# Optimization experiments

Hardware: AMD Instinct MI355X
Metric: run time of the kernel (lower is better)

## Reference

```python
import jax, jax.numpy as jnp
import numpy as np

B, K, D = 512, 36, 1024
N_KERNELS = 4
OUT_DIM = 1024
OUT_PER_KERNEL = OUT_DIM // N_KERNELS  # 256


def setup_inputs() -> dict:
    key = jax.random.key(0)
    k1, k2, k3, k4, k5 = jax.random.split(key, 5)
    neighbourhood_features = jax.random.normal(k1, (B, K, D), dtype=jnp.float32)
    region_relation_weights = jax.random.uniform(k2, (B, K, K), dtype=jnp.float32)
    # Gaussian mixture params: init uniform(0, 1) as in init_parameters()
    mean_relation = jax.random.uniform(k3, (N_KERNELS,), dtype=jnp.float32)
    precision_relation = jax.random.uniform(k4, (N_KERNELS,), dtype=jnp.float32)
    # Per-kernel Linear weights (bias=False), torch default init U(-1/sqrt(D), 1/sqrt(D))
    bound = 1.0 / np.sqrt(D)
    W = jax.random.uniform(k5, (N_KERNELS, OUT_PER_KERNEL, D), dtype=jnp.float32,
                           minval=-bound, maxval=bound)
    return {
        "neighbourhood_features": neighbourhood_features,
        "region_relation_weights": region_relation_weights,
        "mean_relation": mean_relation,
        "precision_relation": precision_relation,
        "W": W,
    }


def reference(neighbourhood_features, region_relation_weights, mean_relation,
              precision_relation, W):
    b, k, d = neighbourhood_features.shape
    # Gaussian mixture edge weights, normalized over kernels: [B,K,K,n_kernels]
    diff = (region_relation_weights[..., None] - mean_relation) ** 2
    w = jnp.exp(-0.5 * diff / (1e-14 + precision_relation ** 2))
    w = w / jnp.sum(w, axis=-1, keepdims=True)
    # Original repeats feat[b,i] over the neighbour axis j, so
    # bmm(w^T, repeated_feat)[b,i,k,:] == (sum_j w[b,i,j,k]) * feat[b,i,:].
    # Exploit that linearity instead of materializing the [B,K,K,D] repeat.
    ws = jnp.sum(w, axis=2)  # [B,K,n_kernels]
    weighted = ws[..., None] * neighbourhood_features[:, :, None, :]  # [B,K,n,D]
    # Per-kernel linear (stacked): [B,K,n_kernels,out_per_kernel]
    out = jnp.einsum('bknd,nod->bkno', weighted, W)
    # Concatenate kernel outputs -> [B,K,out_feat_dim]
    return out.reshape(b, k, -1)
```

## Files before the change

kernel.cpp:

```cpp
#include <hip/hip_runtime.h>
#include <stdint.h>

#define BB   512
#define KNB  36
#define DD   1024
#define MM   (BB*KNB)
#define NN   1024

typedef float  f32x4  __attribute__((ext_vector_type(4)));
typedef __bf16 bf16x8 __attribute__((ext_vector_type(8)));
typedef unsigned short u16;
typedef unsigned int   u32;

__device__ __forceinline__ u16 f2bf(float f) {
    u32 u = __float_as_uint(f);
    u32 r = (u + 0x7fffu + ((u >> 16) & 1u)) >> 16;
    return (u16)r;
}

__device__ __forceinline__ void gld16(const void* g, void* l) {
    __builtin_amdgcn_global_load_lds(
        (const __attribute__((address_space(1))) u32*)g,
        (__attribute__((address_space(3))) u32*)l,
        16, 0, 0);
}

__device__ __forceinline__ void cast_chunk_swz(const float* __restrict__ in,
                                               u16* __restrict__ out,
                                               long long c, int r) {
    long long src = (c & ~7LL) | ((c & 7) ^ (r & 7));
    const f32x4* p = (const f32x4*)(in + src * 8);
    f32x4 v0 = p[0], v1 = p[1];
    union { u16 us[8]; uint4 u4; } pk;
    pk.us[0] = f2bf(v0.x); pk.us[1] = f2bf(v0.y);
    pk.us[2] = f2bf(v0.z); pk.us[3] = f2bf(v0.w);
    pk.us[4] = f2bf(v1.x); pk.us[5] = f2bf(v1.y);
    pk.us[6] = f2bf(v1.z); pk.us[7] = f2bf(v1.w);
    *((uint4*)(out + c * 8)) = pk.u4;
}

#define WS_BLOCKS   72
#define CW_BLOCKS   512
#define CA_BLOCKS   1152
#define CA_THREADS  (CA_BLOCKS * 256)
__global__ void prep_kernel(const float* __restrict__ rrw,
                            const float* __restrict__ mean,
                            const float* __restrict__ prec,
                            float* __restrict__ wsT,
                            const float* __restrict__ W,
                            u16* __restrict__ Wbf,
                            const float* __restrict__ A,
                            u16* __restrict__ Abf) {
    const int blk = blockIdx.x;
    if (blk < WS_BLOCKS) {
        int id = blk * 256 + threadIdx.x;
        float m0 = mean[0], m1 = mean[1], m2 = mean[2], m3 = mean[3];
        float i0 = 1.0f / (1e-14f + prec[0] * prec[0]);
        float i1 = 1.0f / (1e-14f + prec[1] * prec[1]);
        float i2 = 1.0f / (1e-14f + prec[2] * prec[2]);
        float i3 = 1.0f / (1e-14f + prec[3] * prec[3]);
        const float* p = rrw + (size_t)id * KNB;
        float a0 = 0.f, a1 = 0.f, a2 = 0.f, a3 = 0.f;
        for (int j = 0; j < KNB; ++j) {
            float x = p[j];
            float d0 = x - m0, d1 = x - m1, d2 = x - m2, d3 = x - m3;
            float e0 = expf(-0.5f * d0 * d0 * i0);
            float e1 = expf(-0.5f * d1 * d1 * i1);
            float e2 = expf(-0.5f * d2 * d2 * i2);
            float e3 = expf(-0.5f * d3 * d3 * i3);
            float inv = 1.0f / (e0 + e1 + e2 + e3);
            a0 += e0 * inv; a1 += e1 * inv; a2 += e2 * inv; a3 += e3 * inv;
        }
        wsT[0 * MM + id] = a0;
        wsT[1 * MM + id] = a1;
        wsT[2 * MM + id] = a2;
        wsT[3 * MM + id] = a3;
    } else if (blk < WS_BLOCKS + CW_BLOCKS) {
        long long c = (long long)(blk - WS_BLOCKS) * 256 + threadIdx.x;
        int r = (int)(c >> 7);
        cast_chunk_swz(W, Wbf, c, r);
    } else {
        long long t = (long long)(blk - WS_BLOCKS - CW_BLOCKS) * 256 + threadIdx.x;
#pragma unroll
        for (int k = 0; k < 8; ++k) {
            long long c = t + (long long)k * CA_THREADS;
            int r = (int)(c >> 7);
            cast_chunk_swz(A, Abf, c, r);
        }
    }
}

#define BM 128
#define BN 128
#define BK 64
#define KTILES (DD / BK)

__global__ __launch_bounds__(256, 4) void gemm_kernel(
        const u16* __restrict__ A,
        const u16* __restrict__ Bm,
        const float* __restrict__ wsT,
        float* __restrict__ out) {
    __shared__ __align__(16) u16 As[BM * BK];
    __shared__ __align__(16) u16 Bs[BN * BK];

    const int tid = threadIdx.x;
    const int bid   = blockIdx.x;
    const int xcd   = bid & 7;
    const int local = bid >> 3;
    const int by    = xcd * 18 + (local >> 3);
    const int bx    = local & 7;
    const int rowBase = by * BM;
    const int colBase = bx * BN;
    const int lane = tid & 63;
    const int w    = tid >> 6;
    const int wr   = w >> 1;
    const int wc   = w & 1;
    const int fr   = lane & 15;
    const int fq   = lane >> 4;

    f32x4 acc[4][4];
#pragma unroll
    for (int m = 0; m < 4; ++m)
#pragma unroll
        for (int n = 0; n < 4; ++n)
            acc[m][n] = (f32x4)0.0f;

    const u16* aptr = A  + (size_t)(rowBase + (tid >> 3)) * DD + (tid & 7) * 8;
    const u16* bptr = Bm + (size_t)(colBase + (tid >> 3)) * DD + (tid & 7) * 8;

    for (int kt = 0; kt < KTILES; ++kt) {
        if (kt) __syncthreads();
#pragma unroll
        for (int i = 0; i < 4; ++i) {
            gld16(aptr + (size_t)i * 32 * DD + kt * BK, &As[(i * 256 + tid) * 8]);
            gld16(bptr + (size_t)i * 32 * DD + kt * BK, &Bs[(i * 256 + tid) * 8]);
        }
        __syncthreads();

#pragma unroll
        for (int kk = 0; kk < 2; ++kk) {
            bf16x8 af[4], bfv[4];
#pragma unroll
            for (int m = 0; m < 4; ++m) {
                int r = wr * 64 + m * 16 + fr;
                int g = kk * 4 + fq;
                af[m] = ((const bf16x8*)&As[r * BK])[g ^ (r & 7)];
            }
#pragma unroll
            for (int n = 0; n < 4; ++n) {
                int r = wc * 64 + n * 16 + fr;
                int g = kk * 4 + fq;
                bfv[n] = ((const bf16x8*)&Bs[r * BK])[g ^ (r & 7)];
            }
#pragma unroll
            for (int m = 0; m < 4; ++m)
#pragma unroll
                for (int n = 0; n < 4; ++n)
                    acc[m][n] = __builtin_amdgcn_mfma_f32_16x16x32_bf16(
                        af[m], bfv[n], acc[m][n], 0, 0, 0);
        }
    }

    const int kn = bx >> 1;
#pragma unroll
    for (int m = 0; m < 4; ++m) {
        int r0 = rowBase + wr * 64 + m * 16 + fq * 4;
        f32x4 s = *(const f32x4*)&wsT[(size_t)kn * MM + r0];
#pragma unroll
        for (int n = 0; n < 4; ++n) {
            int c = colBase + wc * 64 + n * 16 + fr;
            float* o = out + (size_t)r0 * NN + c;
            o[0 * NN] = acc[m][n][0] * s[0];
            o[1 * NN] = acc[m][n][1] * s[1];
            o[2 * NN] = acc[m][n][2] * s[2];
            o[3 * NN] = acc[m][n][3] * s[3];
        }
    }
}

extern "C" void kernel_launch(void* const* d_in, const int* in_sizes, int n_in,
                              void* d_out, int out_size, void* d_ws, size_t ws_size,
                              hipStream_t stream) {
    const float* feat = (const float*)d_in[0];
    const float* rrw  = (const float*)d_in[1];
    const float* mean = (const float*)d_in[2];
    const float* prec = (const float*)d_in[3];
    const float* W    = (const float*)d_in[4];
    float* out = (float*)d_out;

    char* ws = (char*)d_ws;
    float* wsT = (float*)ws;
    u16*   Wbf = (u16*)(ws + 294912);
    u16*   Abf = (u16*)(ws + 294912 + 2097152);

    prep_kernel<<<dim3(WS_BLOCKS + CW_BLOCKS + CA_BLOCKS), dim3(256), 0, stream>>>(
        rrw, mean, prec, wsT, W, Wbf, feat, Abf);
    gemm_kernel<<<dim3((MM / BM) * (NN / BN)), dim3(256), 0, stream>>>(Abf, Wbf, wsT, out);
}
```

Before: 73.88 us.

## Fuse fp32-to-bf16 activation cast into GEMM A-tile loading

Removes the separate pass that converted the feature matrix to bf16 in the prep kernel. The GEMM now loads fp32 A tiles into registers, converts them to bf16 and writes them into swizzled LDS, while B still uses direct global-to-LDS loads. This saves a full write and re-read of the bf16 activation copy. In exchange each GEMM block reads twice the A bytes, and each of the 8 column blocks re-reads the same fp32 rows. The load sits right before the barrier with no overlap, and the occupancy hint drops from 4 to 3.

```diff
diff --git a/kernel.cpp b/kernel.cpp
--- a/kernel.cpp
+++ b/kernel.cpp
@@ -23,6 +23,13 @@
         (const __attribute__((address_space(1))) u32*)g,
         (__attribute__((address_space(3))) u32*)l,
         16, 0, 0);
+}
+
+__device__ __forceinline__ bf16x8 cvt8(f32x4 lo, f32x4 hi) {
+    bf16x8 r;
+    r[0] = (__bf16)lo.x; r[1] = (__bf16)lo.y; r[2] = (__bf16)lo.z; r[3] = (__bf16)lo.w;
+    r[4] = (__bf16)hi.x; r[5] = (__bf16)hi.y; r[6] = (__bf16)hi.z; r[7] = (__bf16)hi.w;
+    return r;
 }
 
 __device__ __forceinline__ void cast_chunk_swz(const float* __restrict__ in,
@@ -41,16 +48,12 @@
 
 #define WS_BLOCKS   72
 #define CW_BLOCKS   512
-#define CA_BLOCKS   1152
-#define CA_THREADS  (CA_BLOCKS * 256)
 __global__ void prep_kernel(const float* __restrict__ rrw,
                             const float* __restrict__ mean,
                             const float* __restrict__ prec,
                             float* __restrict__ wsT,
                             const float* __restrict__ W,
-                            u16* __restrict__ Wbf,
-                            const float* __restrict__ A,
-                            u16* __restrict__ Abf) {
+                            u16* __restrict__ Wbf) {
     const int blk = blockIdx.x;
     if (blk < WS_BLOCKS) {
         int id = blk * 256 + threadIdx.x;
@@ -75,18 +78,10 @@
         wsT[1 * MM + id] = a1;
         wsT[2 * MM + id] = a2;
         wsT[3 * MM + id] = a3;
-    } else if (blk < WS_BLOCKS + CW_BLOCKS) {
+    } else {
         long long c = (long long)(blk - WS_BLOCKS) * 256 + threadIdx.x;
         int r = (int)(c >> 7);
         cast_chunk_swz(W, Wbf, c, r);
-    } else {
-        long long t = (long long)(blk - WS_BLOCKS - CW_BLOCKS) * 256 + threadIdx.x;
-#pragma unroll
-        for (int k = 0; k < 8; ++k) {
-            long long c = t + (long long)k * CA_THREADS;
-            int r = (int)(c >> 7);
-            cast_chunk_swz(A, Abf, c, r);
-        }
     }
 }
 
@@ -95,8 +90,8 @@
 #define BK 64
 #define KTILES (DD / BK)
 
-__global__ __launch_bounds__(256, 4) void gemm_kernel(
-        const u16* __restrict__ A,
+__global__ __launch_bounds__(256, 3) void gemm_kernel(
+        const float* __restrict__ A,
         const u16* __restrict__ Bm,
         const float* __restrict__ wsT,
         float* __restrict__ out) {
@@ -125,18 +120,35 @@
         for (int n = 0; n < 4; ++n)
             acc[m][n] = (f32x4)0.0f;
 
-    const u16* aptr = A  + (size_t)(rowBase + (tid >> 3)) * DD + (tid & 7) * 8;
-    const u16* bptr = Bm + (size_t)(colBase + (tid >> 3)) * DD + (tid & 7) * 8;
-
-    for (int kt = 0; kt < KTILES; ++kt) {
-        if (kt) __syncthreads();
+    const int ar0 = tid >> 3;
+    const int aj  = tid & 7;
+    const float* abase = A + (size_t)(rowBase + ar0) * DD + aj * 8;
+    const u16*   bptr  = Bm + (size_t)(colBase + ar0) * DD + aj * 8;
+
+    f32x4 ra[4][2];
+
+    auto ISSUE_A = [&](int kt) {
 #pragma unroll
         for (int i = 0; i < 4; ++i) {
-            gld16(aptr + (size_t)i * 32 * DD + kt * BK, &As[(i * 256 + tid) * 8]);
+            const float* src = abase + (size_t)i * 32 * DD + kt * BK;
+            ra[i][0] = *(const f32x4*)src;
+            ra[i][1] = *(const f32x4*)(src + 4);
+        }
+    };
+    auto ISSUE_B = [&](int kt) {
+#pragma unroll
+        for (int i = 0; i < 4; ++i)
             gld16(bptr + (size_t)i * 32 * DD + kt * BK, &Bs[(i * 256 + tid) * 8]);
-        }
-        __syncthreads();
-
+    };
+    auto WRITE_A = [&]() {
+#pragma unroll
+        for (int i = 0; i < 4; ++i) {
+            int r = i * 32 + ar0;
+            *(bf16x8*)&As[r * BK + (aj ^ (r & 7)) * 8] = cvt8(ra[i][0], ra[i][1]);
+        }
+    };
+
+    auto COMPUTE = [&]() {
 #pragma unroll
         for (int kk = 0; kk < 2; ++kk) {
             bf16x8 af[4], bfv[4];
@@ -158,6 +170,22 @@
                 for (int n = 0; n < 4; ++n)
                     acc[m][n] = __builtin_amdgcn_mfma_f32_16x16x32_bf16(
                         af[m], bfv[n], acc[m][n], 0, 0, 0);
+        }
+    };
+
+    ISSUE_A(0);
+    ISSUE_B(0);
+    WRITE_A();
+    __syncthreads();
+
+    for (int kt = 0; kt < KTILES; ++kt) {
+        COMPUTE();
+        if (kt + 1 < KTILES) {
+            __syncthreads();
+            ISSUE_A(kt + 1);
+            ISSUE_B(kt + 1);
+            WRITE_A();
+            __syncthreads();
         }
     }
 
@@ -191,9 +219,8 @@
     char* ws = (char*)d_ws;
     float* wsT = (float*)ws;
     u16*   Wbf = (u16*)(ws + 294912);
-    u16*   Abf = (u16*)(ws + 294912 + 2097152);
-
-    prep_kernel<<<dim3(WS_BLOCKS + CW_BLOCKS + CA_BLOCKS), dim3(256), 0, stream>>>(
-        rrw, mean, prec, wsT, W, Wbf, feat, Abf);
-    gemm_kernel<<<dim3((MM / BM) * (NN / BN)), dim3(256), 0, stream>>>(Abf, Wbf, wsT, out);
-}
+
+    prep_kernel<<<dim3(WS_BLOCKS + CW_BLOCKS), dim3(256), 0, stream>>>(
+        rrw, mean, prec, wsT, W, Wbf);
+    gemm_kernel<<<dim3((MM / BM) * (NN / BN)), dim3(256), 0, stream>>>(feat, Wbf, wsT, out);
+}
```

After: 81.32 us. 1.1x slower.
